# Kernel optimization log

Measured on AMD Instinct MI355X. Metric: run time of the kernel, lower is better.

Reference implementation:

```python
import jax, jax.numpy as jnp
import numpy as np

EMBED_DIM = 1024
NUM_HEADS = 16
HEAD_DIM = EMBED_DIM // NUM_HEADS


def setup_inputs() -> dict:
    key = jax.random.key(0)
    kx, kq, kk, kv, ko = jax.random.split(key, 5)
    scale = 1.0 / np.sqrt(EMBED_DIM)
    return {
        "x": jax.random.normal(kx, (4, 2048, EMBED_DIM), dtype=jnp.float32),
        # nn.Linear weights are [out, in]; y = x @ W.T
        "w_q": jax.random.normal(kq, (EMBED_DIM, EMBED_DIM), dtype=jnp.float32) * scale,
        "w_k": jax.random.normal(kk, (EMBED_DIM, EMBED_DIM), dtype=jnp.float32) * scale,
        "w_v": jax.random.normal(kv, (EMBED_DIM, EMBED_DIM), dtype=jnp.float32) * scale,
        "w_o": jax.random.normal(ko, (EMBED_DIM, EMBED_DIM), dtype=jnp.float32) * scale,
    }


def reference(x, w_q, w_k, w_v, w_o):
    b, s, _ = x.shape
    # projections (Linear with no bias: x @ W.T)
    q = (x @ w_q.T).reshape(b, s, NUM_HEADS, HEAD_DIM).transpose(0, 2, 1, 3)
    k = (x @ w_k.T).reshape(b, s, NUM_HEADS, HEAD_DIM).transpose(0, 2, 1, 3)
    v = (x @ w_v.T).reshape(b, s, NUM_HEADS, HEAD_DIM).transpose(0, 2, 1, 3)
    # scores: [b, h, s, s]
    scores = jnp.einsum("bhqd,bhkd->bhqk", q, k) / jnp.sqrt(jnp.float32(HEAD_DIM)).astype(x.dtype)
    attn = jax.nn.softmax(scores, axis=-1)
    out = jnp.einsum("bhqk,bhkd->bhqd", attn, v)  # [b, h, s, d]
    out = out.transpose(0, 2, 1, 3).reshape(b, s, EMBED_DIM)
    return out @ w_o.T
```

## Files before the change

### kernel.cpp

```cpp
#include <hip/hip_runtime.h>
#include <math.h>

#define EMBED 1024
#define NHEAD 16
#define HDIM  64
#define BATCH 4
#define SEQ   2048
#define MROWS (BATCH * SEQ)

typedef __attribute__((ext_vector_type(8))) short short8;
typedef __attribute__((ext_vector_type(4))) float floatx4;
typedef __attribute__((ext_vector_type(16))) float floatx16;

#if __has_builtin(__builtin_amdgcn_exp2f)
#define EXP2(x) __builtin_amdgcn_exp2f(x)
#else
#define EXP2(x) exp2f(x)
#endif

__device__ __forceinline__ unsigned short f2bf(float f) {
  unsigned u = __float_as_uint(f);
  u += 0x7fffu + ((u >> 16) & 1u);
  return (unsigned short)(u >> 16);
}

#if __has_builtin(__builtin_amdgcn_cvt_pk_bf16_f32)
__device__ __forceinline__ unsigned pack2bf(float lo, float hi) {
  typedef __attribute__((ext_vector_type(2))) __bf16 bf2;
  union { bf2 b; unsigned u; } c;
  c.b = __builtin_amdgcn_cvt_pk_bf16_f32(lo, hi);
  return c.u;
}
#else
__device__ __forceinline__ unsigned pack2bf(float lo, float hi) {
  return ((__float_as_uint(lo) + 0x8000u) >> 16) |
         ((__float_as_uint(hi) + 0x8000u) & 0xffff0000u);
}
#endif

__device__ __forceinline__ void gl_lds16(const void* g, void* l) {
  __builtin_amdgcn_global_load_lds(
      (const __attribute__((address_space(1))) unsigned int*)g,
      (__attribute__((address_space(3))) unsigned int*)l, 16, 0, 0);
}

__global__ __launch_bounds__(256) void cast_bf16_kernel(
    const float* __restrict__ x,  const float* __restrict__ wq,
    const float* __restrict__ wk, const float* __restrict__ wv,
    const float* __restrict__ wo,
    unsigned short* __restrict__ xb, unsigned short* __restrict__ wb) {
  const size_t NX = (size_t)MROWS * EMBED;
  size_t i4 = ((size_t)blockIdx.x * 256 + threadIdx.x) * 4;
  const float* src;
  unsigned short* dst;
  size_t off;
  if (i4 < NX) {
    src = x; dst = xb; off = i4;
  } else {
    size_t j = i4 - NX;
    int r = (int)(j >> 20);
    off = j & ((1u << 20) - 1);
    src = (r == 0) ? wq : (r == 1) ? wk : (r == 2) ? wv : wo;
    dst = wb + ((size_t)r << 20);
  }
  float4 v = *(const float4*)(src + off);
  ushort4 o;
  o.x = f2bf(v.x); o.y = f2bf(v.y); o.z = f2bf(v.z); o.w = f2bf(v.w);
  *(ushort4*)(dst + off) = o;
}

__device__ __forceinline__ void gemm_core(
    const unsigned short* __restrict__ Amat,
    const unsigned short* __restrict__ Bmat,
    int mBase, int nBase,
    unsigned short* As, unsigned short* Bs,
    floatx4 acc[4][4]) {
  const int t = threadIdx.x;
  const int lane = t & 63, w = t >> 6;
  const int wr = w >> 1, wc = w & 1;
  const int quad = lane >> 4, l15 = lane & 15;

  const int f0 = (w * 2 + 0) * 64 + lane;
  const int f1 = (w * 2 + 1) * 64 + lane;
  const unsigned short* ga0 = Amat + (size_t)(mBase + (f0 >> 2)) * EMBED + (f0 & 3) * 8;
  const unsigned short* ga1 = Amat + (size_t)(mBase + (f1 >> 2)) * EMBED + (f1 & 3) * 8;
  const unsigned short* gb0 = Bmat + (size_t)(nBase + (f0 >> 2)) * EMBED + (f0 & 3) * 8;
  const unsigned short* gb1 = Bmat + (size_t)(nBase + (f1 >> 2)) * EMBED + (f1 & 3) * 8;
  unsigned short* la0 = As + (w * 2 + 0) * 512;
  unsigned short* la1 = As + (w * 2 + 1) * 512;
  unsigned short* lb0 = Bs + (w * 2 + 0) * 512;
  unsigned short* lb1 = Bs + (w * 2 + 1) * 512;

  for (int kb = 0; kb < EMBED; kb += 32) {
    __syncthreads();
    gl_lds16(ga0 + kb, la0);
    gl_lds16(ga1 + kb, la1);
    gl_lds16(gb0 + kb, lb0);
    gl_lds16(gb1 + kb, lb1);
    __syncthreads();
    short8 a[4], b[4];
#pragma unroll
    for (int mi = 0; mi < 4; ++mi)
      a[mi] = *(const short8*)&As[(wr * 64 + mi * 16 + l15) * 32 + quad * 8];
#pragma unroll
    for (int ni = 0; ni < 4; ++ni)
      b[ni] = *(const short8*)&Bs[(wc * 64 + ni * 16 + l15) * 32 + quad * 8];
#pragma unroll
    for (int mi = 0; mi < 4; ++mi)
#pragma unroll
      for (int ni = 0; ni < 4; ++ni)
        acc[mi][ni] = __builtin_amdgcn_mfma_f32_16x16x32_bf16(
            a[mi], b[ni], acc[mi][ni], 0, 0, 0);
  }
}

__global__ __launch_bounds__(256) void proj_qkv_bf16(
    const unsigned short* __restrict__ xb,
    const unsigned short* __restrict__ wb,
    unsigned short* __restrict__ qkv) {
  const int which = blockIdx.z;
  const unsigned short* W = wb + ((size_t)which << 20);
  const int nBase = blockIdx.x * 128;
  const int mBase = blockIdx.y * 128;

  __shared__ unsigned short As[128 * 32];
  __shared__ unsigned short Bs[128 * 32];

  floatx4 acc[4][4] = {};
  gemm_core(xb, W, mBase, nBase, As, Bs, acc);

  const int t = threadIdx.x;
  const int lane = t & 63, w = t >> 6;
  const int wr = w >> 1, wc = w & 1;
  const int quad = lane >> 4, l15 = lane & 15;

  unsigned short* out = qkv + (size_t)which * MROWS * EMBED;
  if (which < 2) {
    const float scale = (which == 0) ? 0.18033688f : 1.0f;
#pragma unroll
    for (int mi = 0; mi < 4; ++mi)
#pragma unroll
      for (int ni = 0; ni < 4; ++ni) {
        const int n = nBase + wc * 64 + ni * 16 + l15;
        const int h = n >> 6, d = n & 63;
#pragma unroll
        for (int r = 0; r < 4; ++r) {
          const int m = mBase + wr * 64 + mi * 16 + quad * 4 + r;
          const int b = m >> 11, s = m & (SEQ - 1);
          out[(((size_t)(b * NHEAD + h) * SEQ) + s) * HDIM + d] =
              f2bf(acc[mi][ni][r] * scale);
        }
      }
  } else {
#pragma unroll
    for (int mi = 0; mi < 4; ++mi) {
      const int m0 = mBase + wr * 64 + mi * 16 + quad * 4;
      const int b = m0 >> 11, s0 = m0 & (SEQ - 1);
#pragma unroll
      for (int ni = 0; ni < 4; ++ni) {
        const int n = nBase + wc * 64 + ni * 16 + l15;
        const int h = n >> 6, d = n & 63;
        ushort4 pk;
        pk.x = f2bf(acc[mi][ni][0]); pk.y = f2bf(acc[mi][ni][1]);
        pk.z = f2bf(acc[mi][ni][2]); pk.w = f2bf(acc[mi][ni][3]);
        *(ushort4*)&out[((size_t)(b * NHEAD + h) * HDIM + d) * SEQ + s0] = pk;
      }
    }
  }
}

__global__ __launch_bounds__(256) void attn_mfma(
    const unsigned short* __restrict__ qkv,
    unsigned short* __restrict__ aout) {
  const unsigned short* Q = qkv;
  const unsigned short* K = qkv + (size_t)MROWS * EMBED;
  const unsigned short* V = qkv + 2 * (size_t)MROWS * EMBED;

  const int id = blockIdx.x;
  const int xcd = id & 7, slot = id >> 3;
  const int bh = xcd * 8 + (slot >> 4);
  const int qBase = (slot & 15) * 128;

  __shared__ unsigned short Ks[128 * 64];
  __shared__ unsigned short Vs[64 * 128];

  const int t = threadIdx.x;
  const int lane = t & 63, w = t >> 6;
  const int h2 = lane >> 5;
  const int q31 = lane & 31;

  const unsigned short* qrow =
      Q + ((size_t)bh * SEQ + qBase + w * 32 + q31) * HDIM;
  short8 qa[4];
#pragma unroll
  for (int ds = 0; ds < 4; ++ds)
    qa[ds] = *(const short8*)(qrow + ds * 16 + h2 * 8);

  const unsigned short* kbase = K + (size_t)bh * SEQ * HDIM;
  const unsigned short* vbase = V + (size_t)bh * HDIM * SEQ;
  const unsigned short* gk[4];
  const unsigned short* gv[4];
  unsigned short* lk[4];
  unsigned short* lv[4];
#pragma unroll
  for (int i = 0; i < 4; ++i) {
    const int c = (w * 4 + i) * 64 + lane;
    const int krow = c >> 3, kgrp = (c & 7) ^ (krow & 7);
    gk[i] = kbase + (size_t)krow * HDIM + kgrp * 8;
    const int vd = c >> 4, vj = (c & 15) ^ (vd & 15);
    gv[i] = vbase + (size_t)vd * SEQ + vj * 8;
    lk[i] = Ks + (w * 4 + i) * 512;
    lv[i] = Vs + (w * 4 + i) * 512;
  }

  floatx16 ot0 = {}, ot1 = {};
  floatx16 osum = {};

  const short one_bf = (short)0x3F80;
  const short8 onesA = {one_bf, one_bf, one_bf, one_bf,
                        one_bf, one_bf, one_bf, one_bf};

  for (int kt = 0; kt < SEQ; kt += 128) {
    __syncthreads();
#pragma unroll
    for (int i = 0; i < 4; ++i) {
      gl_lds16(gk[i] + (size_t)kt * HDIM, lk[i]);
      gl_lds16(gv[i] + kt, lv[i]);
    }
    __syncthreads();

#pragma unroll
    for (int sub = 0; sub < 2; ++sub) {
      const int koff = sub * 64;

      floatx16 st0 = {}, st1 = {};
#pragma unroll
      for (int ds = 0; ds < 4; ++ds) {
        const int g = ds * 2 + h2;
        const int k0 = koff + q31;
        short8 ka0 = *(const short8*)&Ks[k0 * 64 + ((g ^ (q31 & 7)) * 8)];
        st0 = __builtin_amdgcn_mfma_f32_32x32x16_bf16(ka0, qa[ds], st0, 0, 0, 0);
        const int k1 = koff + 32 + q31;
        short8 ka1 = *(const short8*)&Ks[k1 * 64 + ((g ^ (q31 & 7)) * 8)];
        st1 = __builtin_amdgcn_mfma_f32_32x32x16_bf16(ka1, qa[ds], st1, 0, 0, 0);
      }

      unsigned pk0[8], pk1[8], sw0[8], sw1[8];
#pragma unroll
      for (int i = 0; i < 8; ++i) {
        pk0[i] = pack2bf(EXP2(st0[2 * i]), EXP2(st0[2 * i + 1]));
        sw0[i] = __shfl_xor(pk0[i], 32);
        pk1[i] = pack2bf(EXP2(st1[2 * i]), EXP2(st1[2 * i + 1]));
        sw1[i] = __shfl_xor(pk1[i], 32);
      }

#pragma unroll
      for (int kst = 0; kst < 4; ++kst) {
        const unsigned* pk = (kst < 2) ? pk0 : pk1;
        const unsigned* sw = (kst < 2) ? sw0 : sw1;
        const int kl = kst & 1;
        union { unsigned u[4]; short8 s; } pb;
        pb.u[0] = h2 ? sw[4 * kl + 2] : pk[4 * kl + 0];
        pb.u[1] = h2 ? sw[4 * kl + 3] : pk[4 * kl + 1];
        pb.u[2] = h2 ? pk[4 * kl + 2] : sw[4 * kl + 0];
        pb.u[3] = h2 ? pk[4 * kl + 3] : sw[4 * kl + 1];

        osum = __builtin_amdgcn_mfma_f32_32x32x16_bf16(onesA, pb.s, osum, 0, 0, 0);

        const int j = sub * 8 + kst * 2 + h2;
        short8 va0 = *(const short8*)&Vs[q31 * 128 + ((j ^ (q31 & 15)) * 8)];
        ot0 = __builtin_amdgcn_mfma_f32_32x32x16_bf16(va0, pb.s, ot0, 0, 0, 0);
        const int d1 = 32 + q31;
        short8 va1 = *(const short8*)&Vs[d1 * 128 + ((j ^ (d1 & 15)) * 8)];
        ot1 = __builtin_amdgcn_mfma_f32_32x32x16_bf16(va1, pb.s, ot1, 0, 0, 0);
      }
    }
  }

  const float inv = 1.0f / osum[0];

  const int b = bh >> 4, hh = bh & 15;
  unsigned short* orow =
      aout + ((size_t)b * SEQ + qBase + w * 32 + q31) * EMBED + hh * HDIM;
#pragma unroll
  for (int rg = 0; rg < 4; ++rg) {
    const int d0 = rg * 8 + h2 * 4;
    ushort4 p0, p1;
    p0.x = f2bf(ot0[4 * rg + 0] * inv); p0.y = f2bf(ot0[4 * rg + 1] * inv);
    p0.z = f2bf(ot0[4 * rg + 2] * inv); p0.w = f2bf(ot0[4 * rg + 3] * inv);
    *(ushort4*)(orow + d0) = p0;
    p1.x = f2bf(ot1[4 * rg + 0] * inv); p1.y = f2bf(ot1[4 * rg + 1] * inv);
    p1.z = f2bf(ot1[4 * rg + 2] * inv); p1.w = f2bf(ot1[4 * rg + 3] * inv);
    *(ushort4*)(orow + 32 + d0) = p1;
  }
}

__global__ __launch_bounds__(256) void out_proj_bf16(
    const unsigned short* __restrict__ aout,
    const unsigned short* __restrict__ wb,
    float* __restrict__ Cout) {
  const int nBase = blockIdx.x * 128;
  const int mBase = blockIdx.y * 128;

  __shared__ unsigned short As[128 * 32];
  __shared__ unsigned short Bs[128 * 32];

  floatx4 acc[4][4] = {};
  gemm_core(aout, wb + ((size_t)3 << 20), mBase, nBase, As, Bs, acc);

  const int t = threadIdx.x;
  const int lane = t & 63, w = t >> 6;
  const int wr = w >> 1, wc = w & 1;
  const int quad = lane >> 4, l15 = lane & 15;

#pragma unroll
  for (int mi = 0; mi < 4; ++mi)
#pragma unroll
    for (int ni = 0; ni < 4; ++ni) {
      const int n = nBase + wc * 64 + ni * 16 + l15;
#pragma unroll
      for (int r = 0; r < 4; ++r) {
        const int m = mBase + wr * 64 + mi * 16 + quad * 4 + r;
        Cout[(size_t)m * EMBED + n] = acc[mi][ni][r];
      }
    }
}

extern "C" void kernel_launch(void* const* d_in, const int* in_sizes, int n_in,
                              void* d_out, int out_size, void* d_ws, size_t ws_size,
                              hipStream_t stream) {
  const float* x  = (const float*)d_in[0];
  const float* wq = (const float*)d_in[1];
  const float* wk = (const float*)d_in[2];
  const float* wv = (const float*)d_in[3];
  const float* wo = (const float*)d_in[4];
  float* out = (float*)d_out;

  char* ws = (char*)d_ws;
  unsigned short* xb   = (unsigned short*)(ws);
  unsigned short* wb   = (unsigned short*)(ws + (16u << 20));
  unsigned short* qkv  = (unsigned short*)(ws + (26u << 20));
  unsigned short* aout = (unsigned short*)(ws + (76u << 20));

  cast_bf16_kernel<<<12288, 256, 0, stream>>>(x, wq, wk, wv, wo, xb, wb);
  proj_qkv_bf16<<<dim3(EMBED / 128, MROWS / 128, 3), 256, 0, stream>>>(xb, wb, qkv);
  attn_mfma<<<1024, 256, 0, stream>>>(qkv, aout);
  out_proj_bf16<<<dim3(EMBED / 128, MROWS / 128), 256, 0, stream>>>(aout, wb, out);
}
```

Before: 316.0 us.

## Replace ones-MFMA row sum with scalar accumulation and use K=8 MFMA for PV

Drops the extra MFMA that multiplied by a ones matrix to get softmax row sums and instead sums the fp32 exponentials in a per-lane scalar, combined across half-waves with one shuffle at the end. The P·V product now uses the 32x32x8 bf16 MFMA so the score accumulator layout feeds the B operand directly, which removes the cross-lane shuffles of packed P. This cuts MFMA and shuffle work per tile. In exchange it issues twice as many smaller MFMAs and smaller V LDS reads, and the row sum is now taken from unrounded fp32 values rather than the bf16 P.

```diff
diff --git a/kernel.cpp b/kernel.cpp
--- a/kernel.cpp
+++ b/kernel.cpp
@@ -8,6 +8,7 @@
 #define SEQ   2048
 #define MROWS (BATCH * SEQ)
 
+typedef __attribute__((ext_vector_type(4))) short short4v;
 typedef __attribute__((ext_vector_type(8))) short short8;
 typedef __attribute__((ext_vector_type(4))) float floatx4;
 typedef __attribute__((ext_vector_type(16))) float floatx16;
@@ -214,11 +215,7 @@
   }
 
   floatx16 ot0 = {}, ot1 = {};
-  floatx16 osum = {};
-
-  const short one_bf = (short)0x3F80;
-  const short8 onesA = {one_bf, one_bf, one_bf, one_bf,
-                        one_bf, one_bf, one_bf, one_bf};
+  float lacc = 0.0f;
 
   for (int kt = 0; kt < SEQ; kt += 128) {
     __syncthreads();
@@ -245,39 +242,40 @@
         st1 = __builtin_amdgcn_mfma_f32_32x32x16_bf16(ka1, qa[ds], st1, 0, 0, 0);
       }
 
-      unsigned pk0[8], pk1[8], sw0[8], sw1[8];
+      float e0[16], e1[16];
+#pragma unroll
+      for (int i = 0; i < 16; ++i) {
+        e0[i] = EXP2(st0[i]);
+        e1[i] = EXP2(st1[i]);
+        lacc += e0[i] + e1[i];
+      }
+      unsigned pk0[8], pk1[8];
 #pragma unroll
       for (int i = 0; i < 8; ++i) {
-        pk0[i] = pack2bf(EXP2(st0[2 * i]), EXP2(st0[2 * i + 1]));
-        sw0[i] = __shfl_xor(pk0[i], 32);
-        pk1[i] = pack2bf(EXP2(st1[2 * i]), EXP2(st1[2 * i + 1]));
-        sw1[i] = __shfl_xor(pk1[i], 32);
-      }
-
-#pragma unroll
-      for (int kst = 0; kst < 4; ++kst) {
-        const unsigned* pk = (kst < 2) ? pk0 : pk1;
-        const unsigned* sw = (kst < 2) ? sw0 : sw1;
-        const int kl = kst & 1;
-        union { unsigned u[4]; short8 s; } pb;
-        pb.u[0] = h2 ? sw[4 * kl + 2] : pk[4 * kl + 0];
-        pb.u[1] = h2 ? sw[4 * kl + 3] : pk[4 * kl + 1];
-        pb.u[2] = h2 ? pk[4 * kl + 2] : sw[4 * kl + 0];
-        pb.u[3] = h2 ? pk[4 * kl + 3] : sw[4 * kl + 1];
-
-        osum = __builtin_amdgcn_mfma_f32_32x32x16_bf16(onesA, pb.s, osum, 0, 0, 0);
-
-        const int j = sub * 8 + kst * 2 + h2;
-        short8 va0 = *(const short8*)&Vs[q31 * 128 + ((j ^ (q31 & 15)) * 8)];
-        ot0 = __builtin_amdgcn_mfma_f32_32x32x16_bf16(va0, pb.s, ot0, 0, 0, 0);
-        const int d1 = 32 + q31;
-        short8 va1 = *(const short8*)&Vs[d1 * 128 + ((j ^ (d1 & 15)) * 8)];
-        ot1 = __builtin_amdgcn_mfma_f32_32x32x16_bf16(va1, pb.s, ot1, 0, 0, 0);
+        pk0[i] = pack2bf(e0[2 * i], e0[2 * i + 1]);
+        pk1[i] = pack2bf(e1[2 * i], e1[2 * i + 1]);
+      }
+
+#pragma unroll
+      for (int s = 0; s < 8; ++s) {
+        const unsigned* pk = (s < 4) ? pk0 : pk1;
+        const int rg = s & 3;
+        union { unsigned u[2]; short4v v; } pb;
+        pb.u[0] = pk[2 * rg + 0];
+        pb.u[1] = pk[2 * rg + 1];
+
+        const int g = sub * 8 + s;
+        const int pos = ((g ^ (q31 & 15)) * 8) + h2 * 4;
+        short4v va0 = *(const short4v*)&Vs[q31 * 128 + pos];
+        ot0 = __builtin_amdgcn_mfma_f32_32x32x8bf16_1k(va0, pb.v, ot0, 0, 0, 0);
+        short4v va1 = *(const short4v*)&Vs[(32 + q31) * 128 + pos];
+        ot1 = __builtin_amdgcn_mfma_f32_32x32x8bf16_1k(va1, pb.v, ot1, 0, 0, 0);
       }
     }
   }
 
-  const float inv = 1.0f / osum[0];
+  const float tot = lacc + __shfl_xor(lacc, 32);
+  const float inv = 1.0f / tot;
 
   const int b = bh >> 4, hh = bh & 15;
   unsigned short* orow =
```

Result: faster. 301.1 us (-4.7%).
